# Performance work log

Hardware: AMD Instinct MI355X
Metric: run time of the kernel (lower is better)

Reference implementation:

```python
import jax, jax.numpy as jnp
import numpy as np

T, H, E, I, K = 4096, 2048, 8, 1408, 2


def setup_inputs() -> dict:
    key = jax.random.key(0)
    k1, k2, k3, k4 = jax.random.split(key, 4)
    x = jax.random.normal(k1, (T, H), dtype=jnp.float32)
    router_w = jax.random.normal(k2, (H, E), dtype=jnp.float32) * 0.02
    gate_up_proj = jax.random.normal(k3, (E, H, 2 * I), dtype=jnp.float32) * 0.02
    down_proj = jax.random.normal(k4, (E, I, H), dtype=jnp.float32) * 0.02
    return {"x": x, "router_w": router_w, "gate_up_proj": gate_up_proj, "down_proj": down_proj}


def _moe_forward(x, router_w, gate_up_proj, down_proj):
    # --- Router: softmax over experts, top-k selection (Qwen2-MoE style) ---
    logits = x @ router_w                                  # [T, E]
    probs = jax.nn.softmax(logits, axis=-1)
    topk_w, topk_idx = jax.lax.top_k(probs, K)             # [T, K]

    # --- Permute: replicate tokens per selected expert, stable-sort by expert id ---
    flat_eid = topk_idx.reshape(-1)                        # [T*K]
    rep_x = jnp.repeat(x, K, axis=0)                       # [T*K, H]
    sort_idx = jnp.argsort(flat_eid, stable=True)          # token permute (like ops.permute)
    perm_x = rep_x[sort_idx]                               # [T*K, H] grouped by expert
    perm_eid = flat_eid[sort_idx]                          # [T*K]

    # --- Grouped expert MLP (gate_up GEMM -> SiLU*up -> down GEMM) ---
    # Faithful to grouped-GEMM math; expressed as a fixed loop over E experts
    # with row masking to stay jit-compatible (no data-dependent shapes).
    out = jnp.zeros_like(perm_x)
    for e in range(E):
        gu = perm_x @ gate_up_proj[e]                      # [T*K, 2I]
        gate, up = gu[:, :I], gu[:, I:]
        h = (jax.nn.silu(gate) * up) @ down_proj[e]        # [T*K, H]
        out = out + jnp.where((perm_eid == e)[:, None], h, 0.0)

    # --- Unpermute + weighted combine over top-k ---
    inv_sort = jnp.argsort(sort_idx)                       # inverse permute mapping
    unperm = out[inv_sort].reshape(T, K, H)
    return jnp.einsum('tkh,tk->th', unperm, topk_w)        # [T, H]


def reference(x, router_w, gate_up_proj, down_proj):
    return _moe_forward(x, router_w, gate_up_proj, down_proj)
```

## Files before the change

### kernel.cpp

```cpp
#include <hip/hip_runtime.h>
#include <hip/hip_bf16.h>

#define T_TOK 4096
#define H_DIM 2048
#define E_NUM 8
#define I_DIM 1408
#define RTOT  8192
#define MAXTILES 72

typedef __bf16 bf16x8 __attribute__((ext_vector_type(8)));
typedef float  floatx4 __attribute__((ext_vector_type(4)));

__device__ __forceinline__ unsigned short f2bf(float f) {
  union { float f; unsigned u; } v; v.f = f;
  unsigned r = v.u + 0x7FFFu + ((v.u >> 16) & 1u);
  return (unsigned short)(r >> 16);
}

__device__ __forceinline__ void async16(const void* g, void* l) {
  __builtin_amdgcn_global_load_lds(
      (__attribute__((address_space(1))) void*)(g),
      (__attribute__((address_space(3))) void*)(l), 16, 0, 0);
}

__global__ void router_kernel(const float* __restrict__ x, const float* __restrict__ rw,
                              int* __restrict__ topk_idx, float* __restrict__ topk_w,
                              int* __restrict__ counts) {
  int wave = threadIdx.x >> 6, lane = threadIdx.x & 63;
  int t = blockIdx.x * 4 + wave;
  const float* xr = x + (size_t)t * H_DIM;
  float acc[E_NUM];
#pragma unroll
  for (int e = 0; e < E_NUM; e++) acc[e] = 0.f;
  for (int h = lane; h < H_DIM; h += 64) {
    float xv = xr[h];
    const float* wr = rw + h * E_NUM;
#pragma unroll
    for (int e = 0; e < E_NUM; e++) acc[e] += xv * wr[e];
  }
#pragma unroll
  for (int e = 0; e < E_NUM; e++) {
    float v = acc[e];
#pragma unroll
    for (int s = 32; s > 0; s >>= 1) v += __shfl_xor(v, s, 64);
    acc[e] = v;
  }
  if (lane == 0) {
    float mx = acc[0];
#pragma unroll
    for (int e = 1; e < E_NUM; e++) mx = fmaxf(mx, acc[e]);
    float p[E_NUM], s = 0.f;
#pragma unroll
    for (int e = 0; e < E_NUM; e++) { p[e] = __expf(acc[e] - mx); s += p[e]; }
    float inv = 1.0f / s;
    int i0 = 0;
#pragma unroll
    for (int e = 1; e < E_NUM; e++) if (p[e] > p[i0]) i0 = e;
    int i1 = (i0 == 0) ? 1 : 0;
#pragma unroll
    for (int e = 0; e < E_NUM; e++) if (e != i0 && p[e] > p[i1]) i1 = e;
    topk_idx[t * 2]     = i0;
    topk_idx[t * 2 + 1] = i1;
    topk_w[t * 2]       = p[i0] * inv;
    topk_w[t * 2 + 1]   = p[i1] * inv;
    atomicAdd(&counts[i0], 1);
    atomicAdd(&counts[i1], 1);
  }
}

__global__ void scan_kernel(const int* __restrict__ counts, int* __restrict__ offsets,
                            int* __restrict__ cursors, int* __restrict__ tile_e,
                            int* __restrict__ tile_m0, int* __restrict__ tile_end) {
  if (threadIdx.x == 0) {
    int o = 0, nt = 0;
    for (int e = 0; e < E_NUM; e++) {
      offsets[e] = o; cursors[e] = o;
      int c = counts[e];
      for (int m = 0; m < c; m += 128) {
        tile_e[nt] = e; tile_m0[nt] = o + m; tile_end[nt] = o + c; nt++;
      }
      o += c;
    }
    for (; nt < MAXTILES; nt++) tile_e[nt] = -1;
  }
}

__global__ void assign_kernel(const int* __restrict__ topk_idx, int* __restrict__ cursors,
                              int* __restrict__ row_of, int* __restrict__ tok_of) {
  int i = blockIdx.x * blockDim.x + threadIdx.x;
  int e = topk_idx[i];
  int row = atomicAdd(&cursors[e], 1);
  row_of[i] = row;
  tok_of[row] = i >> 1;
}

__global__ void gather_kernel(const float* __restrict__ x, const int* __restrict__ tok_of,
                              unsigned short* __restrict__ Xp) {
  int row = blockIdx.x;
  int t = tok_of[row];
  const float4* src = (const float4*)(x + (size_t)t * H_DIM);
  ushort4* dst = (ushort4*)(Xp + (size_t)row * H_DIM);
  for (int i = threadIdx.x; i < H_DIM / 4; i += 256) {
    float4 v = src[i];
    ushort4 o;
    o.x = f2bf(v.x); o.y = f2bf(v.y); o.z = f2bf(v.z); o.w = f2bf(v.w);
    dst[i] = o;
  }
}

__global__ void convert_gu_kernel(const float* __restrict__ W,
                                  unsigned short* __restrict__ WgT,
                                  unsigned short* __restrict__ WuT) {
  __shared__ unsigned short t[64][72];
  int e = blockIdx.z;
  int k0 = blockIdx.y * 64;
  int n0 = blockIdx.x * 64;
  const float* Wp = W + (size_t)e * H_DIM * (2 * I_DIM);
  int f4 = threadIdx.x & 15, kr = threadIdx.x >> 4;
#pragma unroll
  for (int p = 0; p < 4; p++) {
    int k = kr + p * 16;
    float4 v = *(const float4*)(Wp + (size_t)(k0 + k) * (2 * I_DIM) + n0 + f4 * 4);
    t[f4 * 4 + 0][k] = f2bf(v.x);
    t[f4 * 4 + 1][k] = f2bf(v.y);
    t[f4 * 4 + 2][k] = f2bf(v.z);
    t[f4 * 4 + 3][k] = f2bf(v.w);
  }
  __syncthreads();
  unsigned short* Op;
  int nb = n0;
  if (n0 < I_DIM) Op = WgT + (size_t)e * I_DIM * H_DIM;
  else { Op = WuT + (size_t)e * I_DIM * H_DIM; nb = n0 - I_DIM; }
  int c = threadIdx.x & 15, nr = threadIdx.x >> 4;
#pragma unroll
  for (int p = 0; p < 4; p++) {
    int n = nr + p * 16;
    *(ushort4*)(Op + (size_t)(nb + n) * H_DIM + k0 + c * 4) = *(const ushort4*)&t[n][c * 4];
  }
}

__global__ void convert_dn_kernel(const float* __restrict__ W,
                                  unsigned short* __restrict__ WdT) {
  __shared__ unsigned short t[64][72];
  int e = blockIdx.z;
  int k0 = blockIdx.y * 64;
  int n0 = blockIdx.x * 64;
  const float* Wp = W + (size_t)e * I_DIM * H_DIM;
  int f4 = threadIdx.x & 15, kr = threadIdx.x >> 4;
#pragma unroll
  for (int p = 0; p < 4; p++) {
    int k = kr + p * 16;
    float4 v = *(const float4*)(Wp + (size_t)(k0 + k) * H_DIM + n0 + f4 * 4);
    t[f4 * 4 + 0][k] = f2bf(v.x);
    t[f4 * 4 + 1][k] = f2bf(v.y);
    t[f4 * 4 + 2][k] = f2bf(v.z);
    t[f4 * 4 + 3][k] = f2bf(v.w);
  }
  __syncthreads();
  unsigned short* Op = WdT + (size_t)e * H_DIM * I_DIM;
  int c = threadIdx.x & 15, nr = threadIdx.x >> 4;
#pragma unroll
  for (int p = 0; p < 4; p++) {
    int n = nr + p * 16;
    *(ushort4*)(Op + (size_t)(n0 + n) * I_DIM + k0 + c * 4) = *(const ushort4*)&t[n][c * 4];
  }
}

__global__ __launch_bounds__(256, 2) void gemm1_kernel(
    const unsigned short* __restrict__ Xp,
    const unsigned short* __restrict__ WgT,
    const unsigned short* __restrict__ WuT,
    const int* __restrict__ tile_e, const int* __restrict__ tile_m0,
    const int* __restrict__ tile_end,
    unsigned short* __restrict__ Hmid) {
  int bid = blockIdx.x;
  int xcd = bid & 7, j = bid >> 3;
  int mt, n;
  if (j < 88) {
    int c = j / 44, jj = j % 44;
    n = jj >> 2;
    mt = xcd * 9 + c * 4 + (jj & 3);
  } else {
    mt = xcd * 9 + 8;
    n = j - 88;
  }
  int e = tile_e[mt];
  if (e < 0) return;
  int m0 = tile_m0[mt];
  int row_end = tile_end[mt];
  int n0 = n * 128;

  __shared__ unsigned short sA[128 * 32];
  __shared__ unsigned short sBg[128 * 32];
  __shared__ unsigned short sBu[128 * 32];

  int tid = threadIdx.x;
  int wave = tid >> 6, lane = tid & 63;

  const unsigned short* ga[2];
  const unsigned short* ggt[2];
  const unsigned short* gut[2];
  unsigned short *la[2], *lg[2], *lu[2];
  const size_t wbase = (size_t)e * I_DIM * H_DIM;
#pragma unroll
  for (int r = 0; r < 2; r++) {
    int lin = r * 256 + tid;
    int row = lin >> 2;
    int col = (lin & 3) * 8;
    int am = m0 + row; if (am > RTOT - 1) am = RTOT - 1;
    ga[r]  = Xp  + (size_t)am * H_DIM + col;
    ggt[r] = WgT + wbase + (size_t)(n0 + row) * H_DIM + col;
    gut[r] = WuT + wbase + (size_t)(n0 + row) * H_DIM + col;
    la[r] = sA  + lin * 8;
    lg[r] = sBg + lin * 8;
    lu[r] = sBu + lin * 8;
  }

  floatx4 accg[4][4] = {};
  floatx4 accu[4][4] = {};

  const unsigned short* sAb = sA  + ((wave & 1) * 64 + (lane & 15)) * 32 + (lane >> 4) * 8;
  const unsigned short* sGb = sBg + ((wave >> 1) * 64 + (lane & 15)) * 32 + (lane >> 4) * 8;
  const unsigned short* sUb = sBu + ((wave >> 1) * 64 + (lane & 15)) * 32 + (lane >> 4) * 8;

  for (int kb = 0; kb < H_DIM / 32; kb++) {
    __syncthreads();
#pragma unroll
    for (int r = 0; r < 2; r++) {
      async16(ga[r],  la[r]); ga[r]  += 32;
      async16(ggt[r], lg[r]); ggt[r] += 32;
      async16(gut[r], lu[r]); gut[r] += 32;
    }
    __syncthreads();
    bf16x8 a[4];
#pragma unroll
    for (int mi = 0; mi < 4; mi++) a[mi] = *(const bf16x8*)(sAb + mi * 16 * 32);
#pragma unroll
    for (int ni = 0; ni < 4; ni++) {
      bf16x8 bg = *(const bf16x8*)(sGb + ni * 16 * 32);
      bf16x8 bu = *(const bf16x8*)(sUb + ni * 16 * 32);
#pragma unroll
      for (int mi = 0; mi < 4; mi++) {
        accg[mi][ni] = __builtin_amdgcn_mfma_f32_16x16x32_bf16(a[mi], bg, accg[mi][ni], 0, 0, 0);
        accu[mi][ni] = __builtin_amdgcn_mfma_f32_16x16x32_bf16(a[mi], bu, accu[mi][ni], 0, 0, 0);
      }
    }
  }

  int mrow = m0 + (wave & 1) * 64 + (lane >> 4) * 4;
  int ncol = n0 + (wave >> 1) * 64 + (lane & 15);
#pragma unroll
  for (int mi = 0; mi < 4; mi++) {
#pragma unroll
    for (int r = 0; r < 4; r++) {
      int m = mrow + mi * 16 + r;
      if (m < row_end) {
        size_t base = (size_t)m * I_DIM + ncol;
#pragma unroll
        for (int ni = 0; ni < 4; ni++) {
          float g = accg[mi][ni][r];
          float u = accu[mi][ni][r];
          float s = g / (1.0f + __expf(-g));
          Hmid[base + ni * 16] = f2bf(s * u);
        }
      }
    }
  }
}

__global__ __launch_bounds__(256, 2) void gemm2_kernel(
    const unsigned short* __restrict__ Hmid,
    const unsigned short* __restrict__ WdT,
    const int* __restrict__ tile_e, const int* __restrict__ tile_m0,
    const int* __restrict__ tile_end,
    float* __restrict__ H2) {
  int bid = blockIdx.x;
  int xcd = bid & 7, j = bid >> 3;
  int mt, n;
  if (j < 128) {
    int c = j / 64, jj = j % 64;
    n = jj >> 2;
    mt = xcd * 9 + c * 4 + (jj & 3);
  } else {
    mt = xcd * 9 + 8;
    n = j - 128;
  }
  int e = tile_e[mt];
  if (e < 0) return;
  int m0 = tile_m0[mt];
  int row_end = tile_end[mt];
  int n0 = n * 128;

  __shared__ unsigned short sA[128 * 32];
  __shared__ unsigned short sB[128 * 32];

  int tid = threadIdx.x;
  int wave = tid >> 6, lane = tid & 63;

  const unsigned short* ga[2];
  const unsigned short* gb[2];
  unsigned short *la[2], *lb[2];
  const size_t wbase = (size_t)e * H_DIM * I_DIM;
#pragma unroll
  for (int r = 0; r < 2; r++) {
    int lin = r * 256 + tid;
    int row = lin >> 2;
    int col = (lin & 3) * 8;
    int am = m0 + row; if (am > RTOT - 1) am = RTOT - 1;
    ga[r] = Hmid + (size_t)am * I_DIM + col;
    gb[r] = WdT + wbase + (size_t)(n0 + row) * I_DIM + col;
    la[r] = sA + lin * 8;
    lb[r] = sB + lin * 8;
  }

  floatx4 acc[4][4] = {};

  const unsigned short* sAb = sA + ((wave & 1) * 64 + (lane & 15)) * 32 + (lane >> 4) * 8;
  const unsigned short* sBb = sB + ((wave >> 1) * 64 + (lane & 15)) * 32 + (lane >> 4) * 8;

  for (int kb = 0; kb < I_DIM / 32; kb++) {
    __syncthreads();
#pragma unroll
    for (int r = 0; r < 2; r++) {
      async16(ga[r], la[r]); ga[r] += 32;
      async16(gb[r], lb[r]); gb[r] += 32;
    }
    __syncthreads();
    bf16x8 a[4];
#pragma unroll
    for (int mi = 0; mi < 4; mi++) a[mi] = *(const bf16x8*)(sAb + mi * 16 * 32);
#pragma unroll
    for (int ni = 0; ni < 4; ni++) {
      bf16x8 b = *(const bf16x8*)(sBb + ni * 16 * 32);
#pragma unroll
      for (int mi = 0; mi < 4; mi++)
        acc[mi][ni] = __builtin_amdgcn_mfma_f32_16x16x32_bf16(a[mi], b, acc[mi][ni], 0, 0, 0);
    }
  }

  int mrow = m0 + (wave & 1) * 64 + (lane >> 4) * 4;
  int ncol = n0 + (wave >> 1) * 64 + (lane & 15);
#pragma unroll
  for (int mi = 0; mi < 4; mi++) {
#pragma unroll
    for (int r = 0; r < 4; r++) {
      int m = mrow + mi * 16 + r;
      if (m < row_end) {
        size_t base = (size_t)m * H_DIM + ncol;
#pragma unroll
        for (int ni = 0; ni < 4; ni++) H2[base + ni * 16] = acc[mi][ni][r];
      }
    }
  }
}

__global__ void combine_kernel(const float* __restrict__ H2, const int* __restrict__ row_of,
                               const float* __restrict__ topk_w, float* __restrict__ out) {
  int t = blockIdx.x >> 1;
  int part = blockIdx.x & 1;
  int c = part * 1024 + threadIdx.x * 4;
  int r0 = row_of[t * 2], r1 = row_of[t * 2 + 1];
  float w0 = topk_w[t * 2], w1 = topk_w[t * 2 + 1];
  float4 a = *(const float4*)(H2 + (size_t)r0 * H_DIM + c);
  float4 b = *(const float4*)(H2 + (size_t)r1 * H_DIM + c);
  float4 o;
  o.x = w0 * a.x + w1 * b.x;
  o.y = w0 * a.y + w1 * b.y;
  o.z = w0 * a.z + w1 * b.z;
  o.w = w0 * a.w + w1 * b.w;
  *(float4*)(out + (size_t)t * H_DIM + c) = o;
}

extern "C" void kernel_launch(void* const* d_in, const int* in_sizes, int n_in,
                              void* d_out, int out_size, void* d_ws, size_t ws_size,
                              hipStream_t stream) {
  const float* x   = (const float*)d_in[0];
  const float* rw  = (const float*)d_in[1];
  const float* wgu = (const float*)d_in[2];
  const float* wdn = (const float*)d_in[3];
  float* out = (float*)d_out;

  char* ws = (char*)d_ws;
  size_t off = 0;
  auto alloc = [&](size_t b) {
    char* p = ws + off;
    off = (off + b + 255) & ~(size_t)255;
    return p;
  };
  unsigned short* WgT  = (unsigned short*)alloc((size_t)E_NUM * I_DIM * H_DIM * 2);
  unsigned short* WuT  = (unsigned short*)alloc((size_t)E_NUM * I_DIM * H_DIM * 2);
  unsigned short* WdT  = (unsigned short*)alloc((size_t)E_NUM * H_DIM * I_DIM * 2);
  unsigned short* Xp   = (unsigned short*)alloc((size_t)RTOT * H_DIM * 2);
  unsigned short* Hmid = (unsigned short*)alloc((size_t)RTOT * I_DIM * 2);
  float* H2            = (float*)alloc((size_t)RTOT * H_DIM * 4);
  int*   topk_idx      = (int*)alloc(RTOT * 4);
  float* topk_w        = (float*)alloc(RTOT * 4);
  int*   row_of        = (int*)alloc(RTOT * 4);
  int*   tok_of        = (int*)alloc(RTOT * 4);
  int*   counts        = (int*)alloc(256);
  int*   offsets       = (int*)alloc(256);
  int*   cursors       = (int*)alloc(256);
  int*   tile_e        = (int*)alloc(128 * 4);
  int*   tile_m0       = (int*)alloc(128 * 4);
  int*   tile_end      = (int*)alloc(128 * 4);

  hipMemsetAsync(counts, 0, E_NUM * sizeof(int), stream);

  convert_gu_kernel<<<dim3(44, 32, 8), 256, 0, stream>>>(wgu, WgT, WuT);
  convert_dn_kernel<<<dim3(32, 22, 8), 256, 0, stream>>>(wdn, WdT);
  router_kernel<<<T_TOK / 4, 256, 0, stream>>>(x, rw, topk_idx, topk_w, counts);
  scan_kernel<<<1, 64, 0, stream>>>(counts, offsets, cursors, tile_e, tile_m0, tile_end);
  assign_kernel<<<RTOT / 256, 256, 0, stream>>>(topk_idx, cursors, row_of, tok_of);
  gather_kernel<<<RTOT, 256, 0, stream>>>(x, tok_of, Xp);
  gemm1_kernel<<<8 * 9 * 11, 256, 0, stream>>>(Xp, WgT, WuT, tile_e, tile_m0, tile_end, Hmid);
  gemm2_kernel<<<8 * 9 * 16, 256, 0, stream>>>(Hmid, WdT, tile_e, tile_m0, tile_end, H2);
  combine_kernel<<<T_TOK * 2, 256, 0, stream>>>(H2, row_of, topk_w, out);
}
```

Measured before the change: 773.3 us.

## Restructure MoE GEMMs with 256-row tiles, pre-tiled layouts and multi-stage async pipeline

```diff
diff --git a/kernel.cpp b/kernel.cpp
--- a/kernel.cpp
+++ b/kernel.cpp
@@ -6,10 +6,22 @@
 #define E_NUM 8
 #define I_DIM 1408
 #define RTOT  8192
-#define MAXTILES 72
+#define MAXMT 40
+#define NT1   11
+#define NKT1  64
+#define NT2   8
+#define NKT2  44
+
+#define QBLK  2080
+#define AREG  8320
+#define BUFU  16640
+#define LDSZ  (4 * BUFU * 2)
 
 typedef __bf16 bf16x8 __attribute__((ext_vector_type(8)));
 typedef float  floatx4 __attribute__((ext_vector_type(4)));
+typedef unsigned short ushortx8 __attribute__((ext_vector_type(8)));
+
+#define VMCNT(n) asm volatile("s_waitcnt vmcnt(" #n ")" ::: "memory")
 
 __device__ __forceinline__ unsigned short f2bf(float f) {
   union { float f; unsigned u; } v; v.f = f;
@@ -68,20 +80,18 @@
   }
 }
 
-__global__ void scan_kernel(const int* __restrict__ counts, int* __restrict__ offsets,
-                            int* __restrict__ cursors, int* __restrict__ tile_e,
-                            int* __restrict__ tile_m0, int* __restrict__ tile_end) {
+__global__ void scan_kernel(const int* __restrict__ counts, int* __restrict__ cursors,
+                            int* __restrict__ tile_e, int* __restrict__ tile_end) {
   if (threadIdx.x == 0) {
     int o = 0, nt = 0;
     for (int e = 0; e < E_NUM; e++) {
-      offsets[e] = o; cursors[e] = o;
+      cursors[e] = o;
       int c = counts[e];
-      for (int m = 0; m < c; m += 128) {
-        tile_e[nt] = e; tile_m0[nt] = o + m; tile_end[nt] = o + c; nt++;
-      }
-      o += c;
+      int ntile = (c + 255) >> 8;
+      for (int j = 0; j < ntile; j++) { tile_e[nt] = e; tile_end[nt] = o + c; nt++; }
+      o += ntile << 8;
     }
-    for (; nt < MAXTILES; nt++) tile_e[nt] = -1;
+    for (; nt < MAXMT; nt++) { tile_e[nt] = -1; tile_end[nt] = 0; }
   }
 }
 
@@ -95,260 +105,226 @@
 }
 
 __global__ void gather_kernel(const float* __restrict__ x, const int* __restrict__ tok_of,
+                              const int* __restrict__ tile_e, const int* __restrict__ tile_end,
                               unsigned short* __restrict__ Xp) {
-  int row = blockIdx.x;
-  int t = tok_of[row];
-  const float4* src = (const float4*)(x + (size_t)t * H_DIM);
-  ushort4* dst = (ushort4*)(Xp + (size_t)row * H_DIM);
-  for (int i = threadIdx.x; i < H_DIM / 4; i += 256) {
-    float4 v = src[i];
-    ushort4 o;
-    o.x = f2bf(v.x); o.y = f2bf(v.y); o.z = f2bf(v.z); o.w = f2bf(v.w);
-    dst[i] = o;
-  }
-}
-
-__global__ void convert_gu_kernel(const float* __restrict__ W,
-                                  unsigned short* __restrict__ WgT,
-                                  unsigned short* __restrict__ WuT) {
-  __shared__ unsigned short t[64][72];
-  int e = blockIdx.z;
-  int k0 = blockIdx.y * 64;
-  int n0 = blockIdx.x * 64;
-  const float* Wp = W + (size_t)e * H_DIM * (2 * I_DIM);
-  int f4 = threadIdx.x & 15, kr = threadIdx.x >> 4;
-#pragma unroll
-  for (int p = 0; p < 4; p++) {
-    int k = kr + p * 16;
-    float4 v = *(const float4*)(Wp + (size_t)(k0 + k) * (2 * I_DIM) + n0 + f4 * 4);
-    t[f4 * 4 + 0][k] = f2bf(v.x);
-    t[f4 * 4 + 1][k] = f2bf(v.y);
-    t[f4 * 4 + 2][k] = f2bf(v.z);
-    t[f4 * 4 + 3][k] = f2bf(v.w);
-  }
-  __syncthreads();
-  unsigned short* Op;
-  int nb = n0;
-  if (n0 < I_DIM) Op = WgT + (size_t)e * I_DIM * H_DIM;
-  else { Op = WuT + (size_t)e * I_DIM * H_DIM; nb = n0 - I_DIM; }
-  int c = threadIdx.x & 15, nr = threadIdx.x >> 4;
-#pragma unroll
-  for (int p = 0; p < 4; p++) {
-    int n = nr + p * 16;
-    *(ushort4*)(Op + (size_t)(nb + n) * H_DIM + k0 + c * 4) = *(const ushort4*)&t[n][c * 4];
-  }
-}
-
-__global__ void convert_dn_kernel(const float* __restrict__ W,
-                                  unsigned short* __restrict__ WdT) {
-  __shared__ unsigned short t[64][72];
-  int e = blockIdx.z;
-  int k0 = blockIdx.y * 64;
-  int n0 = blockIdx.x * 64;
-  const float* Wp = W + (size_t)e * I_DIM * H_DIM;
-  int f4 = threadIdx.x & 15, kr = threadIdx.x >> 4;
-#pragma unroll
-  for (int p = 0; p < 4; p++) {
-    int k = kr + p * 16;
-    float4 v = *(const float4*)(Wp + (size_t)(k0 + k) * H_DIM + n0 + f4 * 4);
-    t[f4 * 4 + 0][k] = f2bf(v.x);
-    t[f4 * 4 + 1][k] = f2bf(v.y);
-    t[f4 * 4 + 2][k] = f2bf(v.z);
-    t[f4 * 4 + 3][k] = f2bf(v.w);
-  }
-  __syncthreads();
-  unsigned short* Op = WdT + (size_t)e * H_DIM * I_DIM;
-  int c = threadIdx.x & 15, nr = threadIdx.x >> 4;
-#pragma unroll
-  for (int p = 0; p < 4; p++) {
-    int n = nr + p * 16;
-    *(ushort4*)(Op + (size_t)(n0 + n) * I_DIM + k0 + c * 4) = *(const ushort4*)&t[n][c * 4];
-  }
-}
-
-__global__ __launch_bounds__(256, 2) void gemm1_kernel(
-    const unsigned short* __restrict__ Xp,
-    const unsigned short* __restrict__ WgT,
-    const unsigned short* __restrict__ WuT,
-    const int* __restrict__ tile_e, const int* __restrict__ tile_m0,
-    const int* __restrict__ tile_end,
+  int kt = blockIdx.x;
+  int mt = blockIdx.y;
+  if (tile_e[mt] < 0) return;
+  int r = threadIdx.x;
+  int row = mt * 256 + r;
+  int end = tile_end[mt];
+  int rr = row < end ? row : end - 1;
+  int tok = tok_of[rr];
+  const float4* xr = (const float4*)(x + (size_t)tok * H_DIM + kt * 32);
+  float v[32];
+#pragma unroll
+  for (int p = 0; p < 8; p++) {
+    float4 t4 = xr[p];
+    v[p * 4 + 0] = t4.x; v[p * 4 + 1] = t4.y; v[p * 4 + 2] = t4.z; v[p * 4 + 3] = t4.w;
+  }
+  unsigned short* dst = Xp + ((size_t)mt * NKT1 + kt) * 8192;
+#pragma unroll
+  for (int q = 0; q < 4; q++) {
+    ushortx8 o;
+#pragma unroll
+    for (int j = 0; j < 8; j++) o[j] = f2bf(v[q * 8 + j]);
+    *(ushortx8*)(dst + ((size_t)q * 256 + r) * 8) = o;
+  }
+}
+
+__global__ void convert_gu_kernel(const float* __restrict__ W, unsigned short* __restrict__ W1T) {
+  int kt = blockIdx.x;
+  int nt = blockIdx.y;
+  int e  = blockIdx.z;
+  int r  = threadIdx.x;
+  int n_phys = nt * 256 + r;
+  int b = n_phys >> 4;
+  int src_col = ((b >> 1) << 4) + (n_phys & 15) + ((b & 1) ? I_DIM : 0);
+  const float* src = W + ((size_t)e * H_DIM + (size_t)kt * 32) * (2 * I_DIM) + src_col;
+  float v[32];
+#pragma unroll
+  for (int k = 0; k < 32; k++) v[k] = src[(size_t)k * (2 * I_DIM)];
+  unsigned short* dst = W1T + ((size_t)(e * NT1 + nt) * NKT1 + kt) * 8192;
+#pragma unroll
+  for (int q = 0; q < 4; q++) {
+    ushortx8 o;
+#pragma unroll
+    for (int j = 0; j < 8; j++) o[j] = f2bf(v[q * 8 + j]);
+    *(ushortx8*)(dst + ((size_t)q * 256 + r) * 8) = o;
+  }
+}
+
+__global__ void convert_dn_kernel(const float* __restrict__ W, unsigned short* __restrict__ WdT) {
+  int kt = blockIdx.x;
+  int nt = blockIdx.y;
+  int e  = blockIdx.z;
+  int r  = threadIdx.x;
+  int src_col = nt * 256 + r;
+  const float* src = W + (size_t)e * I_DIM * H_DIM + (size_t)kt * 32 * H_DIM + src_col;
+  float v[32];
+#pragma unroll
+  for (int k = 0; k < 32; k++) v[k] = src[(size_t)k * H_DIM];
+  unsigned short* dst = WdT + ((size_t)(e * NT2 + nt) * NKT2 + kt) * 8192;
+#pragma unroll
+  for (int q = 0; q < 4; q++) {
+    ushortx8 o;
+#pragma unroll
+    for (int j = 0; j < 8; j++) o[j] = f2bf(v[q * 8 + j]);
+    *(ushortx8*)(dst + ((size_t)q * 256 + r) * 8) = o;
+  }
+}
+
+__global__ __launch_bounds__(512, 2) void gemm1_kernel(
+    const unsigned short* __restrict__ Xp, const unsigned short* __restrict__ W1T,
+    const int* __restrict__ tile_e, const int* __restrict__ tile_end,
     unsigned short* __restrict__ Hmid) {
+  extern __shared__ unsigned short sm[];
   int bid = blockIdx.x;
-  int xcd = bid & 7, j = bid >> 3;
-  int mt, n;
-  if (j < 88) {
-    int c = j / 44, jj = j % 44;
-    n = jj >> 2;
-    mt = xcd * 9 + c * 4 + (jj & 3);
-  } else {
-    mt = xcd * 9 + 8;
-    n = j - 88;
-  }
+  int mt = bid % MAXMT, nt = bid / MAXMT;
   int e = tile_e[mt];
   if (e < 0) return;
-  int m0 = tile_m0[mt];
   int row_end = tile_end[mt];
-  int n0 = n * 128;
-
-  __shared__ unsigned short sA[128 * 32];
-  __shared__ unsigned short sBg[128 * 32];
-  __shared__ unsigned short sBu[128 * 32];
-
-  int tid = threadIdx.x;
-  int wave = tid >> 6, lane = tid & 63;
-
-  const unsigned short* ga[2];
-  const unsigned short* ggt[2];
-  const unsigned short* gut[2];
-  unsigned short *la[2], *lg[2], *lu[2];
-  const size_t wbase = (size_t)e * I_DIM * H_DIM;
-#pragma unroll
-  for (int r = 0; r < 2; r++) {
-    int lin = r * 256 + tid;
-    int row = lin >> 2;
-    int col = (lin & 3) * 8;
-    int am = m0 + row; if (am > RTOT - 1) am = RTOT - 1;
-    ga[r]  = Xp  + (size_t)am * H_DIM + col;
-    ggt[r] = WgT + wbase + (size_t)(n0 + row) * H_DIM + col;
-    gut[r] = WuT + wbase + (size_t)(n0 + row) * H_DIM + col;
-    la[r] = sA  + lin * 8;
-    lg[r] = sBg + lin * 8;
-    lu[r] = sBu + lin * 8;
-  }
-
-  floatx4 accg[4][4] = {};
-  floatx4 accu[4][4] = {};
-
-  const unsigned short* sAb = sA  + ((wave & 1) * 64 + (lane & 15)) * 32 + (lane >> 4) * 8;
-  const unsigned short* sGb = sBg + ((wave >> 1) * 64 + (lane & 15)) * 32 + (lane >> 4) * 8;
-  const unsigned short* sUb = sBu + ((wave >> 1) * 64 + (lane & 15)) * 32 + (lane >> 4) * 8;
-
-  for (int kb = 0; kb < H_DIM / 32; kb++) {
-    __syncthreads();
-#pragma unroll
-    for (int r = 0; r < 2; r++) {
-      async16(ga[r],  la[r]); ga[r]  += 32;
-      async16(ggt[r], lg[r]); ggt[r] += 32;
-      async16(gut[r], lu[r]); gut[r] += 32;
-    }
-    __syncthreads();
-    bf16x8 a[4];
-#pragma unroll
-    for (int mi = 0; mi < 4; mi++) a[mi] = *(const bf16x8*)(sAb + mi * 16 * 32);
-#pragma unroll
-    for (int ni = 0; ni < 4; ni++) {
-      bf16x8 bg = *(const bf16x8*)(sGb + ni * 16 * 32);
-      bf16x8 bu = *(const bf16x8*)(sUb + ni * 16 * 32);
-#pragma unroll
-      for (int mi = 0; mi < 4; mi++) {
-        accg[mi][ni] = __builtin_amdgcn_mfma_f32_16x16x32_bf16(a[mi], bg, accg[mi][ni], 0, 0, 0);
-        accu[mi][ni] = __builtin_amdgcn_mfma_f32_16x16x32_bf16(a[mi], bu, accu[mi][ni], 0, 0, 0);
-      }
-    }
-  }
-
-  int mrow = m0 + (wave & 1) * 64 + (lane >> 4) * 4;
-  int ncol = n0 + (wave >> 1) * 64 + (lane & 15);
-#pragma unroll
-  for (int mi = 0; mi < 4; mi++) {
-#pragma unroll
-    for (int r = 0; r < 4; r++) {
-      int m = mrow + mi * 16 + r;
-      if (m < row_end) {
-        size_t base = (size_t)m * I_DIM + ncol;
-#pragma unroll
-        for (int ni = 0; ni < 4; ni++) {
-          float g = accg[mi][ni][r];
-          float u = accu[mi][ni][r];
+  int tid = threadIdx.x, wave = tid >> 6, lane = tid & 63;
+  int wm = wave >> 2, wn = wave & 3;
+  int q = lane >> 4, l15 = lane & 15;
+
+  const unsigned short* gA = Xp  + (size_t)mt * ((size_t)NKT1 * 8192) + tid * 8;
+  const unsigned short* gB = W1T + (size_t)(e * NT1 + nt) * ((size_t)NKT1 * 8192) + tid * 8;
+
+  const int u1 = tid + 512;
+  const int dA0 = tid * 8 + (tid >> 8) * 32;
+  const int dA1 = u1 * 8 + (u1 >> 8) * 32;
+
+  auto STAGE = [&](int buf) {
+    unsigned short* sb = sm + buf * BUFU;
+    async16(gA,        sb + dA0);
+    async16(gA + 4096, sb + dA1);
+    async16(gB,        sb + AREG + dA0);
+    async16(gB + 4096, sb + AREG + dA1);
+    gA += 8192; gB += 8192;
+  };
+
+  STAGE(0); STAGE(1);
+
+  const int off_a = q * QBLK + (wm * 128 + l15) * 8;
+  const int off_b = AREG + q * QBLK + (wn * 64 + l15) * 8;
+
+  floatx4 acc[8][4] = {};
+
+  for (int t = 0; t < NKT1; t++) {
+    if (t + 1 < NKT1) { VMCNT(4); } else { VMCNT(0); }
+    __builtin_amdgcn_s_barrier();
+    __builtin_amdgcn_sched_barrier(0);
+    if (t + 2 < NKT1) STAGE((t + 2) & 3);
+    const unsigned short* base = sm + (t & 3) * BUFU;
+    bf16x8 a[8], b[4];
+#pragma unroll
+    for (int mi = 0; mi < 8; mi++) a[mi] = *(const bf16x8*)(base + off_a + mi * 128);
+#pragma unroll
+    for (int ni = 0; ni < 4; ni++) b[ni] = *(const bf16x8*)(base + off_b + ni * 128);
+    __builtin_amdgcn_s_setprio(1);
+#pragma unroll
+    for (int ni = 0; ni < 4; ni++)
+#pragma unroll
+      for (int mi = 0; mi < 8; mi++)
+        acc[mi][ni] = __builtin_amdgcn_mfma_f32_16x16x32_bf16(a[mi], b[ni], acc[mi][ni], 0, 0, 0);
+    __builtin_amdgcn_s_setprio(0);
+  }
+
+  const int rt_base = wm * 128 + (lane >> 4) * 4;
+  const int lc0 = nt * 128 + wn * 32 + l15;
+  unsigned short* Hb = Hmid + (size_t)mt * ((size_t)NKT2 * 8192);
+  int rend = row_end - mt * 256;
+#pragma unroll
+  for (int mi = 0; mi < 8; mi++) {
+#pragma unroll
+    for (int p = 0; p < 2; p++) {
+      int lcol = lc0 + p * 16;
+      int kt2 = lcol >> 5, q2 = (lcol >> 3) & 3, j2 = lcol & 7;
+      unsigned short* hp = Hb + (size_t)kt2 * 8192 + q2 * 2048 + j2;
+#pragma unroll
+      for (int r = 0; r < 4; r++) {
+        int rt = rt_base + mi * 16 + r;
+        if (rt < rend) {
+          float g = acc[mi][2 * p][r];
+          float u = acc[mi][2 * p + 1][r];
           float s = g / (1.0f + __expf(-g));
-          Hmid[base + ni * 16] = f2bf(s * u);
+          hp[rt * 8] = f2bf(s * u);
         }
       }
     }
   }
 }
 
-__global__ __launch_bounds__(256, 2) void gemm2_kernel(
-    const unsigned short* __restrict__ Hmid,
-    const unsigned short* __restrict__ WdT,
-    const int* __restrict__ tile_e, const int* __restrict__ tile_m0,
-    const int* __restrict__ tile_end,
+__global__ __launch_bounds__(512, 2) void gemm2_kernel(
+    const unsigned short* __restrict__ Hmid, const unsigned short* __restrict__ WdT,
+    const int* __restrict__ tile_e, const int* __restrict__ tile_end,
     float* __restrict__ H2) {
+  extern __shared__ unsigned short sm[];
   int bid = blockIdx.x;
-  int xcd = bid & 7, j = bid >> 3;
-  int mt, n;
-  if (j < 128) {
-    int c = j / 64, jj = j % 64;
-    n = jj >> 2;
-    mt = xcd * 9 + c * 4 + (jj & 3);
-  } else {
-    mt = xcd * 9 + 8;
-    n = j - 128;
-  }
+  int mt = bid % MAXMT, nt = bid / MAXMT;
   int e = tile_e[mt];
   if (e < 0) return;
-  int m0 = tile_m0[mt];
   int row_end = tile_end[mt];
-  int n0 = n * 128;
-
-  __shared__ unsigned short sA[128 * 32];
-  __shared__ unsigned short sB[128 * 32];
-
-  int tid = threadIdx.x;
-  int wave = tid >> 6, lane = tid & 63;
-
-  const unsigned short* ga[2];
-  const unsigned short* gb[2];
-  unsigned short *la[2], *lb[2];
-  const size_t wbase = (size_t)e * H_DIM * I_DIM;
-#pragma unroll
-  for (int r = 0; r < 2; r++) {
-    int lin = r * 256 + tid;
-    int row = lin >> 2;
-    int col = (lin & 3) * 8;
-    int am = m0 + row; if (am > RTOT - 1) am = RTOT - 1;
-    ga[r] = Hmid + (size_t)am * I_DIM + col;
-    gb[r] = WdT + wbase + (size_t)(n0 + row) * I_DIM + col;
-    la[r] = sA + lin * 8;
-    lb[r] = sB + lin * 8;
-  }
-
-  floatx4 acc[4][4] = {};
-
-  const unsigned short* sAb = sA + ((wave & 1) * 64 + (lane & 15)) * 32 + (lane >> 4) * 8;
-  const unsigned short* sBb = sB + ((wave >> 1) * 64 + (lane & 15)) * 32 + (lane >> 4) * 8;
-
-  for (int kb = 0; kb < I_DIM / 32; kb++) {
-    __syncthreads();
-#pragma unroll
-    for (int r = 0; r < 2; r++) {
-      async16(ga[r], la[r]); ga[r] += 32;
-      async16(gb[r], lb[r]); gb[r] += 32;
-    }
-    __syncthreads();
-    bf16x8 a[4];
-#pragma unroll
-    for (int mi = 0; mi < 4; mi++) a[mi] = *(const bf16x8*)(sAb + mi * 16 * 32);
+  int tid = threadIdx.x, wave = tid >> 6, lane = tid & 63;
+  int wm = wave >> 2, wn = wave & 3;
+  int q = lane >> 4, l15 = lane & 15;
+
+  const unsigned short* gA = Hmid + (size_t)mt * ((size_t)NKT2 * 8192) + tid * 8;
+  const unsigned short* gB = WdT  + (size_t)(e * NT2 + nt) * ((size_t)NKT2 * 8192) + tid * 8;
+
+  const int u1 = tid + 512;
+  const int dA0 = tid * 8 + (tid >> 8) * 32;
+  const int dA1 = u1 * 8 + (u1 >> 8) * 32;
+
+  auto STAGE = [&](int buf) {
+    unsigned short* sb = sm + buf * BUFU;
+    async16(gA,        sb + dA0);
+    async16(gA + 4096, sb + dA1);
+    async16(gB,        sb + AREG + dA0);
+    async16(gB + 4096, sb + AREG + dA1);
+    gA += 8192; gB += 8192;
+  };
+
+  STAGE(0); STAGE(1);
+
+  const int off_a = q * QBLK + (wm * 128 + l15) * 8;
+  const int off_b = AREG + q * QBLK + (wn * 64 + l15) * 8;
+
+  floatx4 acc[8][4] = {};
+
+  for (int t = 0; t < NKT2; t++) {
+    if (t + 1 < NKT2) { VMCNT(4); } else { VMCNT(0); }
+    __builtin_amdgcn_s_barrier();
+    __builtin_amdgcn_sched_barrier(0);
+    if (t + 2 < NKT2) STAGE(((unsigned)(t + 2)) & 3);
+    const unsigned short* base = sm + (t & 3) * BUFU;
+    bf16x8 a[8], b[4];
+#pragma unroll
+    for (int mi = 0; mi < 8; mi++) a[mi] = *(const bf16x8*)(base + off_a + mi * 128);
+#pragma unroll
+    for (int ni = 0; ni < 4; ni++) b[ni] = *(const bf16x8*)(base + off_b + ni * 128);
+    __builtin_amdgcn_s_setprio(1);
+#pragma unroll
+    for (int ni = 0; ni < 4; ni++)
+#pragma unroll
+      for (int mi = 0; mi < 8; mi++)
+        acc[mi][ni] = __builtin_amdgcn_mfma_f32_16x16x32_bf16(a[mi], b[ni], acc[mi][ni], 0, 0, 0);
+    __builtin_amdgcn_s_setprio(0);
+  }
+
+  const int rt_base = wm * 128 + (lane >> 4) * 4;
+  const int nb = nt * 256 + wn * 64 + l15;
+  float* H2b = H2 + (size_t)mt * 256 * H_DIM + nb;
+  int rend = row_end - mt * 256;
+#pragma unroll
+  for (int mi = 0; mi < 8; mi++) {
 #pragma unroll
     for (int ni = 0; ni < 4; ni++) {
-      bf16x8 b = *(const bf16x8*)(sBb + ni * 16 * 32);
-#pragma unroll
-      for (int mi = 0; mi < 4; mi++)
-        acc[mi][ni] = __builtin_amdgcn_mfma_f32_16x16x32_bf16(a[mi], b, acc[mi][ni], 0, 0, 0);
-    }
-  }
-
-  int mrow = m0 + (wave & 1) * 64 + (lane >> 4) * 4;
-  int ncol = n0 + (wave >> 1) * 64 + (lane & 15);
-#pragma unroll
-  for (int mi = 0; mi < 4; mi++) {
-#pragma unroll
-    for (int r = 0; r < 4; r++) {
-      int m = mrow + mi * 16 + r;
-      if (m < row_end) {
-        size_t base = (size_t)m * H_DIM + ncol;
-#pragma unroll
-        for (int ni = 0; ni < 4; ni++) H2[base + ni * 16] = acc[mi][ni][r];
+#pragma unroll
+      for (int r = 0; r < 4; r++) {
+        int rt = rt_base + mi * 16 + r;
+        if (rt < rend) H2b[(size_t)rt * H_DIM + ni * 16] = acc[mi][ni][r];
       }
     }
   }
@@ -380,6 +356,15 @@
   const float* wdn = (const float*)d_in[3];
   float* out = (float*)d_out;
 
+  static bool attr_done = false;
+  if (!attr_done) {
+    hipFuncSetAttribute(reinterpret_cast<const void*>(gemm1_kernel),
+                        hipFuncAttributeMaxDynamicSharedMemorySize, LDSZ);
+    hipFuncSetAttribute(reinterpret_cast<const void*>(gemm2_kernel),
+                        hipFuncAttributeMaxDynamicSharedMemorySize, LDSZ);
+    attr_done = true;
+  }
+
   char* ws = (char*)d_ws;
   size_t off = 0;
   auto alloc = [&](size_t b) {
@@ -387,32 +372,29 @@
     off = (off + b + 255) & ~(size_t)255;
     return p;
   };
-  unsigned short* WgT  = (unsigned short*)alloc((size_t)E_NUM * I_DIM * H_DIM * 2);
-  unsigned short* WuT  = (unsigned short*)alloc((size_t)E_NUM * I_DIM * H_DIM * 2);
-  unsigned short* WdT  = (unsigned short*)alloc((size_t)E_NUM * H_DIM * I_DIM * 2);
-  unsigned short* Xp   = (unsigned short*)alloc((size_t)RTOT * H_DIM * 2);
-  unsigned short* Hmid = (unsigned short*)alloc((size_t)RTOT * I_DIM * 2);
-  float* H2            = (float*)alloc((size_t)RTOT * H_DIM * 4);
+  unsigned short* W1T  = (unsigned short*)alloc((size_t)E_NUM * NT1 * NKT1 * 8192 * 2);
+  unsigned short* WdT  = (unsigned short*)alloc((size_t)E_NUM * NT2 * NKT2 * 8192 * 2);
+  unsigned short* Xp   = (unsigned short*)alloc((size_t)MAXMT * NKT1 * 8192 * 2);
+  unsigned short* Hmid = (unsigned short*)alloc((size_t)MAXMT * NKT2 * 8192 * 2);
+  float* H2            = (float*)alloc((size_t)MAXMT * 256 * H_DIM * 4);
   int*   topk_idx      = (int*)alloc(RTOT * 4);
   float* topk_w        = (float*)alloc(RTOT * 4);
   int*   row_of        = (int*)alloc(RTOT * 4);
-  int*   tok_of        = (int*)alloc(RTOT * 4);
+  int*   tok_of        = (int*)alloc((size_t)MAXMT * 256 * 4);
   int*   counts        = (int*)alloc(256);
-  int*   offsets       = (int*)alloc(256);
   int*   cursors       = (int*)alloc(256);
-  int*   tile_e        = (int*)alloc(128 * 4);
-  int*   tile_m0       = (int*)alloc(128 * 4);
-  int*   tile_end      = (int*)alloc(128 * 4);
+  int*   tile_e        = (int*)alloc(64 * 4);
+  int*   tile_end      = (int*)alloc(64 * 4);
 
   hipMemsetAsync(counts, 0, E_NUM * sizeof(int), stream);
 
-  convert_gu_kernel<<<dim3(44, 32, 8), 256, 0, stream>>>(wgu, WgT, WuT);
-  convert_dn_kernel<<<dim3(32, 22, 8), 256, 0, stream>>>(wdn, WdT);
+  convert_gu_kernel<<<dim3(NKT1, NT1, E_NUM), 256, 0, stream>>>(wgu, W1T);
+  convert_dn_kernel<<<dim3(NKT2, NT2, E_NUM), 256, 0, stream>>>(wdn, WdT);
   router_kernel<<<T_TOK / 4, 256, 0, stream>>>(x, rw, topk_idx, topk_w, counts);
-  scan_kernel<<<1, 64, 0, stream>>>(counts, offsets, cursors, tile_e, tile_m0, tile_end);
+  scan_kernel<<<1, 64, 0, stream>>>(counts, cursors, tile_e, tile_end);
   assign_kernel<<<RTOT / 256, 256, 0, stream>>>(topk_idx, cursors, row_of, tok_of);
-  gather_kernel<<<RTOT, 256, 0, stream>>>(x, tok_of, Xp);
-  gemm1_kernel<<<8 * 9 * 11, 256, 0, stream>>>(Xp, WgT, WuT, tile_e, tile_m0, tile_end, Hmid);
-  gemm2_kernel<<<8 * 9 * 16, 256, 0, stream>>>(Hmid, WdT, tile_e, tile_m0, tile_end, H2);
+  gather_kernel<<<dim3(NKT1, MAXMT), 256, 0, stream>>>(x, tok_of, tile_e, tile_end, Xp);
+  gemm1_kernel<<<MAXMT * NT1, 512, LDSZ, stream>>>(Xp, W1T, tile_e, tile_end, Hmid);
+  gemm2_kernel<<<MAXMT * NT2, 512, LDSZ, stream>>>(Hmid, WdT, tile_e, tile_end, H2);
   combine_kernel<<<T_TOK * 2, 256, 0, stream>>>(H2, row_of, topk_w, out);
 }
```

New measurement: 741.5 us. 4.1% less time.
